# Kernel tuning notes

Hardware: AMD Instinct MI355X
Metric: run time of the kernel (lower is better)

The kernel has to match this reference:

```python
import jax, jax.numpy as jnp
import numpy as np

N = 131072      # batch of states
Q = 8           # q_ndim (dof_ndim)
DZ = 2 * Q      # state dim [q, p]
H = 256         # hidden_size
ALPHA_RATIO = 100000.0 / (100000.0 + 100000.0)  # 0.5


def setup_inputs() -> dict:
    key = jax.random.key(0)
    ks = jax.random.split(key, 12)
    def w(i, shape, scale=0.05):
        return jax.random.normal(ks[i], shape, dtype=jnp.float32) * scale
    return {
        "t": jnp.zeros((), jnp.float32),
        "z": jax.random.normal(ks[0], (N, DZ), jnp.float32),
        # h_net hidden layers (the output Linear of h_net only feeds a print, omitted)
        "hW1": w(1, (H, DZ)), "hb1": w(2, (H,)),
        "hW2": w(3, (H, H)), "hb2": w(4, (H,)),
        # flex_net layers
        "fW1": w(5, (H, DZ)), "fb1": w(6, (H,)),
        "fW2": w(7, (H, H)), "fb2": w(8, (H,)),
        "fW3": w(9, (DZ, H)), "fb3": w(10, (DZ,)),
    }


def reference(t, z, hW1, hb1, hW2, hb2, fW1, fb1, fW2, fb2, fW3, fb3):
    ar = ALPHA_RATIO
    # h_net hidden pass; sps[i] = d tanh(a)/da = 1 - tanh(a)^2 (autograd.grad in torch)
    a1 = z @ hW1.T + hb1            # (N, H)
    t1 = jnp.tanh(a1)
    s1 = 1.0 - t1 * t1              # sps[0]
    a2 = t1 @ hW2.T + hb2           # (N, H)
    t2 = jnp.tanh(a2)
    s2 = 1.0 - t2 * t2              # sps[1]
    # flex_net pass, mixing flex activations with h-net tanh derivatives (reversed order)
    f = z @ fW1.T + fb1
    f = (1.0 - ar) * f * s2 + ar * jnp.tanh(f)   # idx = 1 -> sps[1]
    f = f @ fW2.T + fb2
    f = (1.0 - ar) * f * s1 + ar * jnp.tanh(f)   # idx = 0 -> sps[0]
    f = f @ fW3.T + fb3             # (N, DZ)
    # angular_dims is empty -> CosSin is identity -> its batched jacobian D is
    # the identity matrix per sample, so bmm(f[:,None,:], D) == f.
    out = f
    # symplectic J: dz/dt = [dH/dp, -dH/dq]
    dz_dt = jnp.concatenate([out[:, Q:], -out[:, :Q]], axis=-1)
    return dz_dt
```

## Files before the change

kernel.cpp:

```cpp
#include <hip/hip_runtime.h>
#include <hip/hip_bf16.h>
#include <stdint.h>


typedef __attribute__((ext_vector_type(8))) short short8;
typedef __attribute__((ext_vector_type(4))) float floatx4;
typedef __attribute__((ext_vector_type(4))) unsigned int uintx4;

static __device__ __forceinline__ unsigned short f2bf(float x) {
  union { float f; uint32_t u; } v; v.f = x;
  return (unsigned short)((v.u + 0x7FFFu + ((v.u >> 16) & 1u)) >> 16);
}
static __device__ __forceinline__ uint32_t packpair(float a, float b) {
  return (uint32_t)f2bf(a) | ((uint32_t)f2bf(b) << 16);
}
static __device__ __forceinline__ float unpklo(uint32_t u) {
  union { uint32_t u; float f; } v; v.u = u << 16;
  return v.f;
}
static __device__ __forceinline__ float unpkhi(uint32_t u) {
  union { uint32_t u; float f; } v; v.u = u & 0xffff0000u;
  return v.f;
}
static __device__ __forceinline__ float tanh_fast(float x) {
  float cx = fminf(4.0f, fmaxf(-4.0f, x));
  float x2 = cx * cx;
  float num = cx * (135135.0f + x2 * (17325.0f + x2 * (378.0f + x2)));
  float den = 135135.0f + x2 * (62370.0f + x2 * (3150.0f + 28.0f * x2));
  return num * __builtin_amdgcn_rcpf(den);
}
static __device__ __forceinline__ floatx4 mfma16(short8 a, short8 b, floatx4 c) {
  return __builtin_amdgcn_mfma_f32_16x16x32_bf16(a, b, c, 0, 0, 0);
}
static __device__ __forceinline__ short8 asfrag(uintx4 u) {
  union { uintx4 u; short8 s; } v; v.u = u;
  return v.s;
}
static __device__ __forceinline__ void gload_lds16(const unsigned short* g,
                                                   unsigned short* l) {
  __builtin_amdgcn_global_load_lds(
      (const __attribute__((address_space(1))) unsigned int*)g,
      (__attribute__((address_space(3))) unsigned int*)l, 16, 0, 0);
}

__global__ __launch_bounds__(256) void prep_kernel(
    const float* __restrict__ hW1, const float* __restrict__ hW2,
    const float* __restrict__ fW1, const float* __restrict__ fW2,
    const float* __restrict__ fW3, unsigned short* __restrict__ ws) {
  int i = blockIdx.x * 256 + threadIdx.x;
  {
    int ob = i >> 12, s = (i >> 9) & 7, lane = (i >> 3) & 63, j = i & 7;
    int m = ob * 16 + (lane & 15), kg = lane >> 4;
    int k = 32 * s + 16 * (j >> 2) + 4 * kg + (j & 3);
    ws[16384 + i] = f2bf(hW2[m * 256 + k]);
    ws[81920 + i] = f2bf(fW2[m * 256 + k]);
  }
  if (i < 8192) {
    int ob = i >> 9, lane = (i >> 3) & 63, j = i & 7;
    int m = ob * 16 + (lane & 15), kg = lane >> 4;
    unsigned short vh = 0, vf = 0;
    if (kg < 2) { int k = kg * 8 + j; vh = f2bf(hW1[m * 16 + k]); vf = f2bf(fW1[m * 16 + k]); }
    ws[i] = vh;
    ws[8192 + i] = vf;
  }
  if (i < 4096) {
    int s = i >> 9, lane = (i >> 3) & 63, j = i & 7;
    int m = lane & 15, kg = lane >> 4;
    int k = 32 * s + 16 * (j >> 2) + 4 * kg + (j & 3);
    ws[147456 + i] = f2bf(fW3[m * 256 + k]);
  }
}

__global__ __launch_bounds__(256, 2) void flexhnn_kernel(
    const float* __restrict__ z,
    const float* __restrict__ hb1, const float* __restrict__ hb2,
    const float* __restrict__ fb1, const float* __restrict__ fb2,
    const float* __restrict__ fb3,
    const unsigned short* __restrict__ ws,
    float* __restrict__ out) {
  __shared__ uint32_t s1_lds[4][2][32][64];
  __shared__ __align__(16) unsigned short wbuf[2][8][64][8];

  const int tid = threadIdx.x, lane = tid & 63, wave = tid >> 6;
  const int c = lane & 15, kg = lane >> 4;
  const int b0 = (blockIdx.x * 4 + wave) * 32;

  const unsigned short* w1hp = ws;
  const unsigned short* w1fp = ws + 8192;
  const unsigned short* w2hp = ws + 16384;
  const unsigned short* w2fp = ws + 81920;
  const unsigned short* w3fp = ws + 147456;

  const int s0 = wave * 2;

  gload_lds16(w2hp + (s0 * 64 + lane) * 8,       &wbuf[0][s0][0][0]);
  gload_lds16(w2hp + ((s0 + 1) * 64 + lane) * 8, &wbuf[0][s0 + 1][0][0]);

  short8 zf[2];
  zf[0] = (short8){0,0,0,0,0,0,0,0};
  zf[1] = (short8){0,0,0,0,0,0,0,0};
  if (kg < 2) {
#pragma unroll
    for (int st = 0; st < 2; ++st) {
      const float* zr = z + (size_t)(b0 + st * 16 + c) * 16 + kg * 8;
      uintx4 u;
      u.x = packpair(zr[0], zr[1]); u.y = packpair(zr[2], zr[3]);
      u.z = packpair(zr[4], zr[5]); u.w = packpair(zr[6], zr[7]);
      zf[st] = asfrag(u);
    }
  }

  uintx4 t1v[2][8];
#pragma unroll
  for (int ob = 0; ob < 16; ++ob) {
    short8 wf = *reinterpret_cast<const short8*>(w1hp + (ob * 64 + lane) * 8);
    floatx4 bias = *reinterpret_cast<const floatx4*>(hb1 + ob * 16 + kg * 4);
#pragma unroll
    for (int st = 0; st < 2; ++st) {
      floatx4 a = mfma16(wf, zf[st], bias);
      float t0 = tanh_fast(a[0]), t1_ = tanh_fast(a[1]);
      float t2 = tanh_fast(a[2]), t3 = tanh_fast(a[3]);
      t1v[st][ob >> 1][(ob & 1) * 2 + 0] = packpair(t0, t1_);
      t1v[st][ob >> 1][(ob & 1) * 2 + 1] = packpair(t2, t3);
      s1_lds[wave][st][ob * 2 + 0][lane] = packpair(1.0f - t0 * t0, 1.0f - t1_ * t1_);
      s1_lds[wave][st][ob * 2 + 1][lane] = packpair(1.0f - t2 * t2, 1.0f - t3 * t3);
    }
  }
  __syncthreads();

  uintx4 fmv[2][8];
#pragma unroll
  for (int ob = 0; ob < 16; ++ob) {
    {
      const int t = ob + 1;
      const unsigned short* base = (t < 16) ? (w2hp + t * 4096) : (w2fp + (t - 16) * 4096);
      gload_lds16(base + (s0 * 64 + lane) * 8,       &wbuf[t & 1][s0][0][0]);
      gload_lds16(base + ((s0 + 1) * 64 + lane) * 8, &wbuf[t & 1][s0 + 1][0][0]);
    }
    floatx4 b2 = *reinterpret_cast<const floatx4*>(hb2 + ob * 16 + kg * 4);
    floatx4 a[2] = {b2, b2};
#pragma unroll
    for (int s = 0; s < 8; ++s) {
      short8 wf = *reinterpret_cast<const short8*>(&wbuf[ob & 1][s][lane][0]);
      a[0] = mfma16(wf, asfrag(t1v[0][s]), a[0]);
      a[1] = mfma16(wf, asfrag(t1v[1][s]), a[1]);
    }
    short8 w1 = *reinterpret_cast<const short8*>(w1fp + (ob * 64 + lane) * 8);
    floatx4 bf1 = *reinterpret_cast<const floatx4*>(fb1 + ob * 16 + kg * 4);
#pragma unroll
    for (int st = 0; st < 2; ++st) {
      floatx4 f = mfma16(w1, zf[st], bf1);
      float fm[4];
#pragma unroll
      for (int r = 0; r < 4; ++r) {
        float t2 = tanh_fast(a[st][r]);
        float s2 = 1.0f - t2 * t2;
        float fv = f[r];
        fm[r] = 0.5f * (fv * s2 + tanh_fast(fv));
      }
      fmv[st][ob >> 1][(ob & 1) * 2 + 0] = packpair(fm[0], fm[1]);
      fmv[st][ob >> 1][(ob & 1) * 2 + 1] = packpair(fm[2], fm[3]);
    }
    __syncthreads();
  }

  uintx4 gv[2][8];
#pragma unroll
  for (int ob = 0; ob < 16; ++ob) {
    if (ob < 15) {
      const unsigned short* base = w2fp + (ob + 1) * 4096;
      gload_lds16(base + (s0 * 64 + lane) * 8,       &wbuf[(ob + 1) & 1][s0][0][0]);
      gload_lds16(base + ((s0 + 1) * 64 + lane) * 8, &wbuf[(ob + 1) & 1][s0 + 1][0][0]);
    }
    floatx4 bf2 = *reinterpret_cast<const floatx4*>(fb2 + ob * 16 + kg * 4);
    floatx4 a[2] = {bf2, bf2};
#pragma unroll
    for (int s = 0; s < 8; ++s) {
      short8 wf = *reinterpret_cast<const short8*>(&wbuf[ob & 1][s][lane][0]);
      a[0] = mfma16(wf, asfrag(fmv[0][s]), a[0]);
      a[1] = mfma16(wf, asfrag(fmv[1][s]), a[1]);
    }
#pragma unroll
    for (int st = 0; st < 2; ++st) {
      uint32_t sp0 = s1_lds[wave][st][ob * 2 + 0][lane];
      uint32_t sp1 = s1_lds[wave][st][ob * 2 + 1][lane];
      float s1a = unpklo(sp0), s1b = unpkhi(sp0), s1c = unpklo(sp1), s1d = unpkhi(sp1);
      float f0 = a[st][0], f1_ = a[st][1], f2_ = a[st][2], f3 = a[st][3];
      float g0 = 0.5f * (f0 * s1a + tanh_fast(f0));
      float g1 = 0.5f * (f1_ * s1b + tanh_fast(f1_));
      float g2 = 0.5f * (f2_ * s1c + tanh_fast(f2_));
      float g3 = 0.5f * (f3 * s1d + tanh_fast(f3));
      gv[st][ob >> 1][(ob & 1) * 2 + 0] = packpair(g0, g1);
      gv[st][ob >> 1][(ob & 1) * 2 + 1] = packpair(g2, g3);
    }
    if (ob < 15) __syncthreads();
  }

  {
    floatx4 b3 = *reinterpret_cast<const floatx4*>(fb3 + kg * 4);
    floatx4 o[2] = {b3, b3};
#pragma unroll
    for (int s = 0; s < 8; ++s) {
      short8 wf = *reinterpret_cast<const short8*>(w3fp + (s * 64 + lane) * 8);
      o[0] = mfma16(wf, asfrag(gv[0][s]), o[0]);
      o[1] = mfma16(wf, asfrag(gv[1][s]), o[1]);
    }
    const int off = (kg < 2) ? (kg * 4 + 8) : (kg * 4 - 8);
    const float sgn = (kg < 2) ? -1.0f : 1.0f;
#pragma unroll
    for (int st = 0; st < 2; ++st) {
      float4 stv;
      stv.x = sgn * o[st][0]; stv.y = sgn * o[st][1];
      stv.z = sgn * o[st][2]; stv.w = sgn * o[st][3];
      *reinterpret_cast<float4*>(out + (size_t)(b0 + st * 16 + c) * 16 + off) = stv;
    }
  }
}

extern "C" void kernel_launch(void* const* d_in, const int* in_sizes, int n_in,
                              void* d_out, int out_size, void* d_ws, size_t ws_size,
                              hipStream_t stream) {
  const float* z   = (const float*)d_in[1];
  const float* hW1 = (const float*)d_in[2];
  const float* hb1 = (const float*)d_in[3];
  const float* hW2 = (const float*)d_in[4];
  const float* hb2 = (const float*)d_in[5];
  const float* fW1 = (const float*)d_in[6];
  const float* fb1 = (const float*)d_in[7];
  const float* fW2 = (const float*)d_in[8];
  const float* fb2 = (const float*)d_in[9];
  const float* fW3 = (const float*)d_in[10];
  const float* fb3 = (const float*)d_in[11];
  unsigned short* ws = (unsigned short*)d_ws;
  float* out = (float*)d_out;

  hipLaunchKernelGGL(prep_kernel, dim3(256), dim3(256), 0, stream,
                     hW1, hW2, fW1, fW2, fW3, ws);
  hipLaunchKernelGGL(flexhnn_kernel, dim3(1024), dim3(256), 0, stream,
                     z, hb1, hb2, fb1, fb2, fb3, (const unsigned short*)ws, out);
}
```

Baseline: 186.6 us.

## Use 8 waves per block with one 16-row sub-tile per wave

Each block now runs 512 threads (8 waves), and each wave handles 16 batch rows instead of two 16-row sub-tiles. Each wave loads one weight slice per stage into the shared LDS double buffer, so register arrays shrink by half. The aim is to cut register pressure and raise occupancy (launch bounds 512,4) for better latency hiding. The cost is that each LDS weight tile now feeds only one MFMA per wave instead of two, and more waves take part in each per-stage barrier.

```diff
diff --git a/kernel.cpp b/kernel.cpp
--- a/kernel.cpp
+++ b/kernel.cpp
@@ -71,19 +71,19 @@
   }
 }
 
-__global__ __launch_bounds__(256, 2) void flexhnn_kernel(
+__global__ __launch_bounds__(512, 4) void flexhnn_kernel(
     const float* __restrict__ z,
     const float* __restrict__ hb1, const float* __restrict__ hb2,
     const float* __restrict__ fb1, const float* __restrict__ fb2,
     const float* __restrict__ fb3,
     const unsigned short* __restrict__ ws,
     float* __restrict__ out) {
-  __shared__ uint32_t s1_lds[4][2][32][64];
+  __shared__ uint32_t s1_lds[8][32][64];
   __shared__ __align__(16) unsigned short wbuf[2][8][64][8];
 
   const int tid = threadIdx.x, lane = tid & 63, wave = tid >> 6;
   const int c = lane & 15, kg = lane >> 4;
-  const int b0 = (blockIdx.x * 4 + wave) * 32;
+  const int b0 = blockIdx.x * 128 + wave * 16;
 
   const unsigned short* w1hp = ws;
   const unsigned short* w1fp = ws + 8192;
@@ -91,129 +91,100 @@
   const unsigned short* w2fp = ws + 81920;
   const unsigned short* w3fp = ws + 147456;
 
-  const int s0 = wave * 2;
-
-  gload_lds16(w2hp + (s0 * 64 + lane) * 8,       &wbuf[0][s0][0][0]);
-  gload_lds16(w2hp + ((s0 + 1) * 64 + lane) * 8, &wbuf[0][s0 + 1][0][0]);
-
-  short8 zf[2];
-  zf[0] = (short8){0,0,0,0,0,0,0,0};
-  zf[1] = (short8){0,0,0,0,0,0,0,0};
+  gload_lds16(w2hp + (wave * 64 + lane) * 8, &wbuf[0][wave][0][0]);
+
+  short8 zf = (short8){0,0,0,0,0,0,0,0};
   if (kg < 2) {
-#pragma unroll
-    for (int st = 0; st < 2; ++st) {
-      const float* zr = z + (size_t)(b0 + st * 16 + c) * 16 + kg * 8;
-      uintx4 u;
-      u.x = packpair(zr[0], zr[1]); u.y = packpair(zr[2], zr[3]);
-      u.z = packpair(zr[4], zr[5]); u.w = packpair(zr[6], zr[7]);
-      zf[st] = asfrag(u);
-    }
-  }
-
-  uintx4 t1v[2][8];
+    const float* zr = z + (size_t)(b0 + c) * 16 + kg * 8;
+    uintx4 u;
+    u.x = packpair(zr[0], zr[1]); u.y = packpair(zr[2], zr[3]);
+    u.z = packpair(zr[4], zr[5]); u.w = packpair(zr[6], zr[7]);
+    zf = asfrag(u);
+  }
+
+  uintx4 t1v[8];
 #pragma unroll
   for (int ob = 0; ob < 16; ++ob) {
     short8 wf = *reinterpret_cast<const short8*>(w1hp + (ob * 64 + lane) * 8);
     floatx4 bias = *reinterpret_cast<const floatx4*>(hb1 + ob * 16 + kg * 4);
-#pragma unroll
-    for (int st = 0; st < 2; ++st) {
-      floatx4 a = mfma16(wf, zf[st], bias);
-      float t0 = tanh_fast(a[0]), t1_ = tanh_fast(a[1]);
-      float t2 = tanh_fast(a[2]), t3 = tanh_fast(a[3]);
-      t1v[st][ob >> 1][(ob & 1) * 2 + 0] = packpair(t0, t1_);
-      t1v[st][ob >> 1][(ob & 1) * 2 + 1] = packpair(t2, t3);
-      s1_lds[wave][st][ob * 2 + 0][lane] = packpair(1.0f - t0 * t0, 1.0f - t1_ * t1_);
-      s1_lds[wave][st][ob * 2 + 1][lane] = packpair(1.0f - t2 * t2, 1.0f - t3 * t3);
-    }
+    floatx4 a = mfma16(wf, zf, bias);
+    float t0 = tanh_fast(a[0]), t1_ = tanh_fast(a[1]);
+    float t2 = tanh_fast(a[2]), t3 = tanh_fast(a[3]);
+    t1v[ob >> 1][(ob & 1) * 2 + 0] = packpair(t0, t1_);
+    t1v[ob >> 1][(ob & 1) * 2 + 1] = packpair(t2, t3);
+    s1_lds[wave][ob * 2 + 0][lane] = packpair(1.0f - t0 * t0, 1.0f - t1_ * t1_);
+    s1_lds[wave][ob * 2 + 1][lane] = packpair(1.0f - t2 * t2, 1.0f - t3 * t3);
   }
   __syncthreads();
 
-  uintx4 fmv[2][8];
+  uintx4 fmv[8];
 #pragma unroll
   for (int ob = 0; ob < 16; ++ob) {
     {
       const int t = ob + 1;
       const unsigned short* base = (t < 16) ? (w2hp + t * 4096) : (w2fp + (t - 16) * 4096);
-      gload_lds16(base + (s0 * 64 + lane) * 8,       &wbuf[t & 1][s0][0][0]);
-      gload_lds16(base + ((s0 + 1) * 64 + lane) * 8, &wbuf[t & 1][s0 + 1][0][0]);
-    }
-    floatx4 b2 = *reinterpret_cast<const floatx4*>(hb2 + ob * 16 + kg * 4);
-    floatx4 a[2] = {b2, b2};
+      gload_lds16(base + (wave * 64 + lane) * 8, &wbuf[t & 1][wave][0][0]);
+    }
+    floatx4 a = *reinterpret_cast<const floatx4*>(hb2 + ob * 16 + kg * 4);
 #pragma unroll
     for (int s = 0; s < 8; ++s) {
       short8 wf = *reinterpret_cast<const short8*>(&wbuf[ob & 1][s][lane][0]);
-      a[0] = mfma16(wf, asfrag(t1v[0][s]), a[0]);
-      a[1] = mfma16(wf, asfrag(t1v[1][s]), a[1]);
+      a = mfma16(wf, asfrag(t1v[s]), a);
     }
     short8 w1 = *reinterpret_cast<const short8*>(w1fp + (ob * 64 + lane) * 8);
     floatx4 bf1 = *reinterpret_cast<const floatx4*>(fb1 + ob * 16 + kg * 4);
-#pragma unroll
-    for (int st = 0; st < 2; ++st) {
-      floatx4 f = mfma16(w1, zf[st], bf1);
-      float fm[4];
-#pragma unroll
-      for (int r = 0; r < 4; ++r) {
-        float t2 = tanh_fast(a[st][r]);
-        float s2 = 1.0f - t2 * t2;
-        float fv = f[r];
-        fm[r] = 0.5f * (fv * s2 + tanh_fast(fv));
-      }
-      fmv[st][ob >> 1][(ob & 1) * 2 + 0] = packpair(fm[0], fm[1]);
-      fmv[st][ob >> 1][(ob & 1) * 2 + 1] = packpair(fm[2], fm[3]);
-    }
+    floatx4 f = mfma16(w1, zf, bf1);
+    float fm[4];
+#pragma unroll
+    for (int r = 0; r < 4; ++r) {
+      float t2 = tanh_fast(a[r]);
+      float s2 = 1.0f - t2 * t2;
+      float fv = f[r];
+      fm[r] = 0.5f * (fv * s2 + tanh_fast(fv));
+    }
+    fmv[ob >> 1][(ob & 1) * 2 + 0] = packpair(fm[0], fm[1]);
+    fmv[ob >> 1][(ob & 1) * 2 + 1] = packpair(fm[2], fm[3]);
     __syncthreads();
   }
 
-  uintx4 gv[2][8];
+  uintx4 gv[8];
 #pragma unroll
   for (int ob = 0; ob < 16; ++ob) {
     if (ob < 15) {
       const unsigned short* base = w2fp + (ob + 1) * 4096;
-      gload_lds16(base + (s0 * 64 + lane) * 8,       &wbuf[(ob + 1) & 1][s0][0][0]);
-      gload_lds16(base + ((s0 + 1) * 64 + lane) * 8, &wbuf[(ob + 1) & 1][s0 + 1][0][0]);
-    }
-    floatx4 bf2 = *reinterpret_cast<const floatx4*>(fb2 + ob * 16 + kg * 4);
-    floatx4 a[2] = {bf2, bf2};
+      gload_lds16(base + (wave * 64 + lane) * 8, &wbuf[(ob + 1) & 1][wave][0][0]);
+    }
+    floatx4 a = *reinterpret_cast<const floatx4*>(fb2 + ob * 16 + kg * 4);
 #pragma unroll
     for (int s = 0; s < 8; ++s) {
       short8 wf = *reinterpret_cast<const short8*>(&wbuf[ob & 1][s][lane][0]);
-      a[0] = mfma16(wf, asfrag(fmv[0][s]), a[0]);
-      a[1] = mfma16(wf, asfrag(fmv[1][s]), a[1]);
-    }
-#pragma unroll
-    for (int st = 0; st < 2; ++st) {
-      uint32_t sp0 = s1_lds[wave][st][ob * 2 + 0][lane];
-      uint32_t sp1 = s1_lds[wave][st][ob * 2 + 1][lane];
-      float s1a = unpklo(sp0), s1b = unpkhi(sp0), s1c = unpklo(sp1), s1d = unpkhi(sp1);
-      float f0 = a[st][0], f1_ = a[st][1], f2_ = a[st][2], f3 = a[st][3];
-      float g0 = 0.5f * (f0 * s1a + tanh_fast(f0));
-      float g1 = 0.5f * (f1_ * s1b + tanh_fast(f1_));
-      float g2 = 0.5f * (f2_ * s1c + tanh_fast(f2_));
-      float g3 = 0.5f * (f3 * s1d + tanh_fast(f3));
-      gv[st][ob >> 1][(ob & 1) * 2 + 0] = packpair(g0, g1);
-      gv[st][ob >> 1][(ob & 1) * 2 + 1] = packpair(g2, g3);
-    }
+      a = mfma16(wf, asfrag(fmv[s]), a);
+    }
+    uint32_t sp0 = s1_lds[wave][ob * 2 + 0][lane];
+    uint32_t sp1 = s1_lds[wave][ob * 2 + 1][lane];
+    float s1a = unpklo(sp0), s1b = unpkhi(sp0), s1c = unpklo(sp1), s1d = unpkhi(sp1);
+    float g0 = 0.5f * (a[0] * s1a + tanh_fast(a[0]));
+    float g1 = 0.5f * (a[1] * s1b + tanh_fast(a[1]));
+    float g2 = 0.5f * (a[2] * s1c + tanh_fast(a[2]));
+    float g3 = 0.5f * (a[3] * s1d + tanh_fast(a[3]));
+    gv[ob >> 1][(ob & 1) * 2 + 0] = packpair(g0, g1);
+    gv[ob >> 1][(ob & 1) * 2 + 1] = packpair(g2, g3);
     if (ob < 15) __syncthreads();
   }
 
   {
-    floatx4 b3 = *reinterpret_cast<const floatx4*>(fb3 + kg * 4);
-    floatx4 o[2] = {b3, b3};
+    floatx4 o = *reinterpret_cast<const floatx4*>(fb3 + kg * 4);
 #pragma unroll
     for (int s = 0; s < 8; ++s) {
       short8 wf = *reinterpret_cast<const short8*>(w3fp + (s * 64 + lane) * 8);
-      o[0] = mfma16(wf, asfrag(gv[0][s]), o[0]);
-      o[1] = mfma16(wf, asfrag(gv[1][s]), o[1]);
+      o = mfma16(wf, asfrag(gv[s]), o);
     }
     const int off = (kg < 2) ? (kg * 4 + 8) : (kg * 4 - 8);
     const float sgn = (kg < 2) ? -1.0f : 1.0f;
-#pragma unroll
-    for (int st = 0; st < 2; ++st) {
-      float4 stv;
-      stv.x = sgn * o[st][0]; stv.y = sgn * o[st][1];
-      stv.z = sgn * o[st][2]; stv.w = sgn * o[st][3];
-      *reinterpret_cast<float4*>(out + (size_t)(b0 + st * 16 + c) * 16 + off) = stv;
-    }
+    float4 stv;
+    stv.x = sgn * o[0]; stv.y = sgn * o[1];
+    stv.z = sgn * o[2]; stv.w = sgn * o[3];
+    *reinterpret_cast<float4*>(out + (size_t)(b0 + c) * 16 + off) = stv;
   }
 }
 
@@ -236,6 +207,6 @@
 
   hipLaunchKernelGGL(prep_kernel, dim3(256), dim3(256), 0, stream,
                      hW1, hW2, fW1, fW2, fW3, ws);
-  hipLaunchKernelGGL(flexhnn_kernel, dim3(1024), dim3(256), 0, stream,
+  hipLaunchKernelGGL(flexhnn_kernel, dim3(1024), dim3(512), 0, stream,
                      z, hb1, hb2, fb1, fb2, fb3, (const unsigned short*)ws, out);
 }
```

Result: no change. 189.9 us (+1.8%).
